# Performance work log

Hardware: AMD Instinct MI355X
Metric: run time of the kernel (lower is better)

Reference implementation:

```python
import jax, jax.numpy as jnp
import numpy as np

NUM_HEADS = 16
ROPE_THETA = 10000.0
SEQ = 2048
D_MODEL = 2048


def _rope(x):
    # x: (seq, heads, head_dim). Equinox RotaryPositionalEmbedding:
    # rotate_half variant with tiled (non-interleaved) cos/sin.
    S, H, hd = x.shape
    half = hd // 2
    freqs = 1.0 / (ROPE_THETA ** (jnp.arange(0, half, dtype=jnp.float32) * 2.0 / hd))  # (half,)
    t = jnp.arange(S, dtype=jnp.float32)
    angles = jnp.outer(t, freqs)  # (S, half)
    cos = jnp.tile(jnp.cos(angles), (1, 2))[:, None, :]  # (S, 1, hd)
    sin = jnp.tile(jnp.sin(angles), (1, 2))[:, None, :]
    x1, x2 = jnp.split(x, 2, axis=-1)
    rot = jnp.concatenate((-x2, x1), axis=-1)  # rotate_half
    return (x * cos + rot * sin).astype(x.dtype)


def setup_inputs() -> dict:
    key = jax.random.key(0)
    ks = jax.random.split(key, 7)
    mk = lambda k, scale=1.0: (jax.random.normal(k, (SEQ, D_MODEL), dtype=jnp.float32) * scale)
    return {
        "query": mk(ks[0]),
        "key_": mk(ks[1]),
        "value": mk(ks[2]),
        "Wq": jax.random.normal(ks[3], (D_MODEL, D_MODEL), dtype=jnp.float32) / np.sqrt(D_MODEL),
        "Wk": jax.random.normal(ks[4], (D_MODEL, D_MODEL), dtype=jnp.float32) / np.sqrt(D_MODEL),
        "Wv": jax.random.normal(ks[5], (D_MODEL, D_MODEL), dtype=jnp.float32) / np.sqrt(D_MODEL),
        "Wo": jax.random.normal(ks[6], (D_MODEL, D_MODEL), dtype=jnp.float32) / np.sqrt(D_MODEL),
    }


def reference(query, key_, value, Wq, Wk, Wv, Wo):
    S, D = query.shape
    H = NUM_HEADS
    hd = D // H
    # QKV projections (equinox Linear: y = W @ x, vmapped over seq -> x @ W.T)
    q = (query @ Wq.T).reshape(S, H, hd)
    k = (key_ @ Wk.T).reshape(S, H, hd)
    v = (value @ Wv.T).reshape(S, H, hd)
    # Per-head RoPE on q and k
    q = _rope(q)
    k = _rope(k)
    # Causal attention, scale 1/sqrt(head_dim) (dropout_p=0, inference)
    attn = jax.nn.dot_product_attention(q[None], k[None], v[None], is_causal=True)[0]  # (S, H, hd)
    # Output projection
    return attn.reshape(S, D) @ Wo.T
```

## Files before the change

kernel.cpp:

```cpp
#include <hip/hip_runtime.h>

typedef unsigned short u16;
typedef __attribute__((ext_vector_type(8))) __bf16 bf16x8;
typedef __attribute__((ext_vector_type(4))) float f32x4;

#define D_MODEL 2048
#define SEQ 2048
#define NHEAD 16
#define HDIM 128

#define AS1 __attribute__((address_space(1)))
#define AS3 __attribute__((address_space(3)))
#define GL2LDS(g, l) __builtin_amdgcn_global_load_lds((AS1 const void*)(g), (AS3 void*)(l), 16, 0, 0)

__device__ __forceinline__ u16 f2bf(float f) {
  unsigned u = __float_as_uint(f);
  u += 0x7fff + ((u >> 16) & 1);
  return (u16)(u >> 16);
}
__device__ __forceinline__ float bf2f(u16 h) {
  return __uint_as_float(((unsigned)h) << 16);
}
__device__ __forceinline__ float fexp2(float x) {
#if __has_builtin(__builtin_amdgcn_exp2f)
  return __builtin_amdgcn_exp2f(x);
#else
  return __expf(x * 0.69314718055994531f);
#endif
}

__global__ __launch_bounds__(256) void k_cast7(const float* i0, const float* i1, const float* i2,
                                               const float* i3, const float* i4, const float* i5,
                                               const float* i6,
                                               u16* o0, u16* o1, u16* o2, u16* o3, u16* o4,
                                               u16* o5, u16* o6) {
  const float* in; u16* out;
  switch (blockIdx.y) {
    case 0: in = i0; out = o0; break;
    case 1: in = i1; out = o1; break;
    case 2: in = i2; out = o2; break;
    case 3: in = i3; out = o3; break;
    case 4: in = i4; out = o4; break;
    case 5: in = i5; out = o5; break;
    default: in = i6; out = o6; break;
  }
  const int i = blockIdx.x * blockDim.x + threadIdx.x;
  const float4 v = reinterpret_cast<const float4*>(in)[i];
  ushort4 o;
  o.x = f2bf(v.x); o.y = f2bf(v.y); o.z = f2bf(v.z); o.w = f2bf(v.w);
  reinterpret_cast<ushort4*>(out)[i] = o;
}

__device__ __forceinline__ void stage128(const u16* __restrict__ P, u16* dst, int row0, int kt,
                                         int t, int w) {
#pragma unroll
  for (int c = 0; c < 4; ++c) {
    const int r = (c * 2048 + t * 8) >> 6;
    const int ch = ((t & 7) ^ (r & 7)) * 8;
    GL2LDS(P + (size_t)(row0 + r) * D_MODEL + kt + ch, dst + c * 2048 + w * 512);
  }
}
__device__ __forceinline__ void stage64(const u16* __restrict__ P, u16* dst, int row0, int kt,
                                        int t, int w) {
#pragma unroll
  for (int c = 0; c < 2; ++c) {
    const int r = (c * 2048 + t * 8) >> 6;
    const int ch = ((t & 7) ^ (r & 7)) * 8;
    GL2LDS(P + (size_t)(row0 + r) * D_MODEL + kt + ch, dst + c * 2048 + w * 512);
  }
}

__device__ __forceinline__ void gemm_nt_body(const u16* __restrict__ A, const u16* __restrict__ B,
                                             void* __restrict__ C, u16* As0, u16* As1,
                                             u16* Bs0, u16* Bs1, int outmode) {
  const int tn = blockIdx.x, tm = blockIdx.y;
  const int t = threadIdx.x;
  const int lane = t & 63, w = t >> 6;
  const int wr = w >> 1, wc = w & 1;
  const int lrow = lane & 15, g = lane >> 4;
  f32x4 acc[4][4] = {};

  stage128(A, As0, tm * 128, 0, t, w);
  stage128(B, Bs0, tn * 128, 0, t, w);
  __syncthreads();

  u16 *Ar = As0, *Br = Bs0, *Aw = As1, *Bw = Bs1;
#pragma unroll 1
  for (int kt = 0; kt < D_MODEL; kt += 64) {
    if (kt + 64 < D_MODEL) {
      stage128(A, Aw, tm * 128, kt + 64, t, w);
      stage128(B, Bw, tn * 128, kt + 64, t, w);
    }
#pragma unroll
    for (int kk = 0; kk < 2; ++kk) {
      bf16x8 af[4], bfr[4];
#pragma unroll
      for (int i = 0; i < 4; ++i) {
        const int sw = (((kk << 2) + g) ^ (lrow & 7)) * 8;
        af[i]  = *(const bf16x8*)(Ar + (wr * 64 + i * 16 + lrow) * 64 + sw);
        bfr[i] = *(const bf16x8*)(Br + (wc * 64 + i * 16 + lrow) * 64 + sw);
      }
#pragma unroll
      for (int i = 0; i < 4; ++i)
#pragma unroll
        for (int j = 0; j < 4; ++j)
          acc[i][j] = __builtin_amdgcn_mfma_f32_16x16x32_bf16(af[i], bfr[j], acc[i][j], 0, 0, 0);
    }
    __syncthreads();
    u16* tp;
    tp = Ar; Ar = Aw; Aw = tp;
    tp = Br; Br = Bw; Bw = tp;
  }

  const int crow0 = tm * 128 + wr * 64 + (lane >> 4) * 4;
  const int ccol0 = tn * 128 + wc * 64 + lrow;
  if (outmode == 2) {
#pragma unroll
    for (int i = 0; i < 4; ++i)
#pragma unroll
      for (int j = 0; j < 4; ++j) {
        ushort4 o;
        o.x = f2bf(acc[i][j][0]); o.y = f2bf(acc[i][j][1]);
        o.z = f2bf(acc[i][j][2]); o.w = f2bf(acc[i][j][3]);
        *(ushort4*)((u16*)C + (size_t)(ccol0 + j * 16) * D_MODEL + crow0 + i * 16) = o;
      }
  } else {
#pragma unroll
    for (int i = 0; i < 4; ++i)
#pragma unroll
      for (int j = 0; j < 4; ++j)
#pragma unroll
        for (int r = 0; r < 4; ++r)
          ((u16*)C)[(size_t)(crow0 + i * 16 + r) * D_MODEL + ccol0 + j * 16] = f2bf(acc[i][j][r]);
  }
}

__global__ __launch_bounds__(256, 2) void k_gemm_qkv(const u16* Xq, const u16* Xk, const u16* Xv,
                                                     const u16* Wq, const u16* Wk, const u16* Wv,
                                                     u16* Q, u16* K, u16* VT) {
  __shared__ u16 As[2][128 * 64], Bs[2][128 * 64];
  const int z = blockIdx.z;
  const u16* A = (z == 0) ? Xq : (z == 1) ? Xk : Xv;
  const u16* B = (z == 0) ? Wq : (z == 1) ? Wk : Wv;
  u16* C = (z == 0) ? Q : (z == 1) ? K : VT;
  gemm_nt_body(A, B, C, As[0], As[1], Bs[0], Bs[1], (z == 2) ? 2 : 0);
}

__global__ __launch_bounds__(256, 2) void k_gemm_out(const u16* __restrict__ A, const u16* __restrict__ B,
                                                     float* __restrict__ C) {
  __shared__ u16 As[2][128 * 64], Bs[2][64 * 64];
  const int tn = blockIdx.x, tm = blockIdx.y;
  const int t = threadIdx.x;
  const int lane = t & 63, w = t >> 6;
  const int wr = w >> 1, wc = w & 1;
  const int lrow = lane & 15, g = lane >> 4;
  f32x4 acc[4][2] = {};

  stage128(A, As[0], tm * 128, 0, t, w);
  stage64(B, Bs[0], tn * 64, 0, t, w);
  __syncthreads();

  u16 *Ar = As[0], *Br = Bs[0], *Aw = As[1], *Bw = Bs[1];
#pragma unroll 1
  for (int kt = 0; kt < D_MODEL; kt += 64) {
    if (kt + 64 < D_MODEL) {
      stage128(A, Aw, tm * 128, kt + 64, t, w);
      stage64(B, Bw, tn * 64, kt + 64, t, w);
    }
#pragma unroll
    for (int kk = 0; kk < 2; ++kk) {
      bf16x8 af[4], bfr[2];
#pragma unroll
      for (int i = 0; i < 4; ++i) {
        const int sw = (((kk << 2) + g) ^ (lrow & 7)) * 8;
        af[i] = *(const bf16x8*)(Ar + (wr * 64 + i * 16 + lrow) * 64 + sw);
        if (i < 2) bfr[i] = *(const bf16x8*)(Br + (wc * 32 + i * 16 + lrow) * 64 + sw);
      }
#pragma unroll
      for (int i = 0; i < 4; ++i)
#pragma unroll
        for (int j = 0; j < 2; ++j)
          acc[i][j] = __builtin_amdgcn_mfma_f32_16x16x32_bf16(af[i], bfr[j], acc[i][j], 0, 0, 0);
    }
    __syncthreads();
    u16* tp;
    tp = Ar; Ar = Aw; Aw = tp;
    tp = Br; Br = Bw; Bw = tp;
  }
  const int crow0 = tm * 128 + wr * 64 + (lane >> 4) * 4;
  const int ccol0 = tn * 64 + wc * 32 + lrow;
#pragma unroll
  for (int i = 0; i < 4; ++i)
#pragma unroll
    for (int j = 0; j < 2; ++j)
#pragma unroll
      for (int r = 0; r < 4; ++r)
        C[(size_t)(crow0 + i * 16 + r) * D_MODEL + ccol0 + j * 16] = acc[i][j][r];
}

__global__ __launch_bounds__(256) void k_rope(u16* Q, u16* K) {
  const int idx = blockIdx.x * blockDim.x + threadIdx.x;
  u16* X = blockIdx.y ? K : Q;
  const float scale = blockIdx.y ? 1.0f : (1.4426950408889634f * 0.08838834764831845f);
  const int s = idx >> 10;
  const int h = (idx >> 6) & 15;
  const int j = idx & 63;
  const float freq = __expf((float)j * -0.14391156831212787f);
  float sn, cs;
  sincosf((float)s * freq, &sn, &cs);
  const size_t base = (size_t)s * D_MODEL + h * HDIM + j;
  const float x1 = bf2f(X[base]), x2 = bf2f(X[base + 64]);
  X[base]      = f2bf((x1 * cs - x2 * sn) * scale);
  X[base + 64] = f2bf((x2 * cs + x1 * sn) * scale);
}

__global__ __launch_bounds__(256, 2) void k_attn(const u16* __restrict__ Q, const u16* __restrict__ K,
                                                 const u16* __restrict__ VT, u16* __restrict__ O) {
  __shared__ u16 Kb[2][64 * 128];
  __shared__ u16 Vb[2][128 * 64];
  __shared__ u16 Pl[4][32 * 64];
  const int bx = blockIdx.x;
  const int h = bx & 15;
  const int qt = 31 - (bx >> 4);
  const int t = threadIdx.x;
  const int lane = t & 63, w = t >> 6;
  const int mh = w & 1, par = w >> 1;
  const int lrow = lane & 15, g = lane >> 4, lk = g * 8;
  const int qrow0 = qt * 64 + mh * 32;

  bf16x8 qf[2][4];
#pragma unroll
  for (int mi = 0; mi < 2; ++mi)
#pragma unroll
    for (int ks = 0; ks < 4; ++ks)
      qf[mi][ks] = *(const bf16x8*)(Q + (size_t)(qrow0 + mi * 16 + lrow) * D_MODEL + h * HDIM + ks * 32 + lk);

  f32x4 accO[2][8] = {};
  float m_run[2][4], l_run[2][4];
#pragma unroll
  for (int mi = 0; mi < 2; ++mi)
#pragma unroll
    for (int r = 0; r < 4; ++r) { m_run[mi][r] = -1e30f; l_run[mi][r] = 0.f; }

  const int nt = qt + 1;
  const int nss = (nt + 1) >> 1;
#pragma unroll 1
  for (int s = 0; s < nss; ++s) {
    const int t0 = 2 * s;
    const int t1 = (2 * s + 1 < nt) ? 2 * s + 1 : nt - 1;
#pragma unroll
    for (int i = 0; i < 4; ++i) {
      const int rk = w * 16 + i * 4 + (lane >> 4);
      const int ck = lane & 15;
      GL2LDS(K + (size_t)(t0 * 64 + rk) * D_MODEL + h * HDIM + ((ck ^ (rk & 15)) * 8),
             Kb[0] + (w * 16 + i * 4) * 128);
      GL2LDS(K + (size_t)(t1 * 64 + rk) * D_MODEL + h * HDIM + ((ck ^ (rk & 15)) * 8),
             Kb[1] + (w * 16 + i * 4) * 128);
      const int rv = w * 32 + i * 8 + (lane >> 3);
      const int cv = lane & 7;
      GL2LDS(VT + (size_t)(h * HDIM + rv) * D_MODEL + t0 * 64 + ((cv ^ (rv & 7)) * 8),
             Vb[0] + (w * 32 + i * 8) * 64);
      GL2LDS(VT + (size_t)(h * HDIM + rv) * D_MODEL + t1 * 64 + ((cv ^ (rv & 7)) * 8),
             Vb[1] + (w * 32 + i * 8) * 64);
    }
    __syncthreads();

    const int T = 2 * s + par;
    if (T < nt) {
      f32x4 sc[2][4] = {};
#pragma unroll
      for (int ks = 0; ks < 4; ++ks) {
        bf16x8 kf[4];
#pragma unroll
        for (int ni = 0; ni < 4; ++ni)
          kf[ni] = *(const bf16x8*)(&Kb[par][(ni * 16 + lrow) * 128 + ((ks * 4 + g) ^ lrow) * 8]);
#pragma unroll
        for (int mi = 0; mi < 2; ++mi)
#pragma unroll
          for (int ni = 0; ni < 4; ++ni)
            sc[mi][ni] = __builtin_amdgcn_mfma_f32_16x16x32_bf16(qf[mi][ks], kf[ni], sc[mi][ni], 0, 0, 0);
      }

      if (T == qt) {
        const int kv = T * 64;
#pragma unroll
        for (int mi = 0; mi < 2; ++mi)
#pragma unroll
          for (int ni = 0; ni < 4; ++ni) {
            const int colg = kv + ni * 16 + lrow;
#pragma unroll
            for (int r = 0; r < 4; ++r) {
              const int rowg = qrow0 + mi * 16 + g * 4 + r;
              if (colg > rowg) sc[mi][ni][r] = -1e30f;
            }
          }
      }

#pragma unroll
      for (int mi = 0; mi < 2; ++mi)
#pragma unroll
        for (int r = 0; r < 4; ++r) {
          float pm = fmaxf(fmaxf(sc[mi][0][r], sc[mi][1][r]), fmaxf(sc[mi][2][r], sc[mi][3][r]));
          pm = fmaxf(pm, __shfl_xor(pm, 1));
          pm = fmaxf(pm, __shfl_xor(pm, 2));
          pm = fmaxf(pm, __shfl_xor(pm, 4));
          pm = fmaxf(pm, __shfl_xor(pm, 8));
          const float mo = m_run[mi][r];
          const float mn = fmaxf(mo, pm);
          const float sf = fexp2(mo - mn);
          float rs = 0.f;
#pragma unroll
          for (int ni = 0; ni < 4; ++ni) {
            const float p = fexp2(sc[mi][ni][r] - mn);
            sc[mi][ni][r] = p;
            rs += p;
          }
          rs += __shfl_xor(rs, 1);
          rs += __shfl_xor(rs, 2);
          rs += __shfl_xor(rs, 4);
          rs += __shfl_xor(rs, 8);
          l_run[mi][r] = l_run[mi][r] * sf + rs;
          m_run[mi][r] = mn;
#pragma unroll
          for (int dt = 0; dt < 8; ++dt) accO[mi][dt][r] *= sf;
        }

#pragma unroll
      for (int mi = 0; mi < 2; ++mi)
#pragma unroll
        for (int ni = 0; ni < 4; ++ni)
#pragma unroll
          for (int r = 0; r < 4; ++r) {
            const int row = mi * 16 + g * 4 + r;
            const int chnk = (2 * ni + (lrow >> 3)) ^ (row & 7);
            Pl[w][row * 64 + chnk * 8 + (lrow & 7)] = f2bf(sc[mi][ni][r]);
          }
      asm volatile("s_waitcnt lgkmcnt(0)" ::: "memory");

#pragma unroll
      for (int ks2 = 0; ks2 < 2; ++ks2) {
        bf16x8 pf[2];
#pragma unroll
        for (int mi = 0; mi < 2; ++mi) {
          const int row = mi * 16 + lrow;
          pf[mi] = *(const bf16x8*)(&Pl[w][row * 64 + ((ks2 * 4 + g) ^ (row & 7)) * 8]);
        }
#pragma unroll
        for (int dt = 0; dt < 8; ++dt) {
          const int R = dt * 16 + lrow;
          const bf16x8 vf = *(const bf16x8*)(&Vb[par][R * 64 + ((ks2 * 4 + g) ^ (R & 7)) * 8]);
#pragma unroll
          for (int mi = 0; mi < 2; ++mi)
            accO[mi][dt] = __builtin_amdgcn_mfma_f32_16x16x32_bf16(pf[mi], vf, accO[mi][dt], 0, 0, 0);
        }
      }
    }
    __syncthreads();
  }

  float* mrg = (float*)&Kb[0][0];
  float* mlb = (float*)&Vb[0][0];
  if (par == 1) {
#pragma unroll
    for (int mi = 0; mi < 2; ++mi)
#pragma unroll
      for (int dt = 0; dt < 8; ++dt)
#pragma unroll
        for (int r = 0; r < 4; ++r)
          mrg[mh * 4096 + (mi * 16 + g * 4 + r) * 128 + dt * 16 + lrow] = accO[mi][dt][r];
#pragma unroll
    for (int mi = 0; mi < 2; ++mi)
#pragma unroll
      for (int r = 0; r < 4; ++r) {
        const int row = mi * 16 + g * 4 + r;
        mlb[mh * 64 + row * 2]     = m_run[mi][r];
        mlb[mh * 64 + row * 2 + 1] = l_run[mi][r];
      }
  }
  __syncthreads();
  if (par == 0) {
#pragma unroll
    for (int mi = 0; mi < 2; ++mi)
#pragma unroll
      for (int r = 0; r < 4; ++r) {
        const int row = mi * 16 + g * 4 + r;
        const float m1 = mlb[mh * 64 + row * 2];
        const float l1 = mlb[mh * 64 + row * 2 + 1];
        const float mn = fmaxf(m_run[mi][r], m1);
        const float f0 = fexp2(m_run[mi][r] - mn);
        const float f1 = fexp2(m1 - mn);
        const float inv = 1.0f / (l_run[mi][r] * f0 + l1 * f1);
        const size_t grow = (size_t)(qrow0 + row);
#pragma unroll
        for (int dt = 0; dt < 8; ++dt) {
          const float v1 = mrg[mh * 4096 + row * 128 + dt * 16 + lrow];
          O[grow * D_MODEL + h * HDIM + dt * 16 + lrow] =
              f2bf((accO[mi][dt][r] * f0 + v1 * f1) * inv);
        }
      }
  }
}

extern "C" void kernel_launch(void* const* d_in, const int* in_sizes, int n_in,
                              void* d_out, int out_size, void* d_ws, size_t ws_size,
                              hipStream_t stream) {
  const float* query = (const float*)d_in[0];
  const float* key_  = (const float*)d_in[1];
  const float* value = (const float*)d_in[2];
  const float* Wq    = (const float*)d_in[3];
  const float* Wk    = (const float*)d_in[4];
  const float* Wv    = (const float*)d_in[5];
  const float* Wo    = (const float*)d_in[6];
  float* out = (float*)d_out;

  const size_t TS = (size_t)SEQ * D_MODEL;
  u16* ws  = (u16*)d_ws;
  u16* bXq = ws + 0 * TS;
  u16* bXk = ws + 1 * TS;
  u16* bXv = ws + 2 * TS;
  u16* bWq = ws + 3 * TS;
  u16* bWk = ws + 4 * TS;
  u16* bWv = ws + 5 * TS;
  u16* bWo = ws + 6 * TS;
  u16* bQ  = ws + 7 * TS;
  u16* bK  = ws + 8 * TS;
  u16* bVT = ws + 9 * TS;
  u16* bA  = ws + 10 * TS;

  const int n4 = (int)(TS / 4);
  k_cast7<<<dim3(n4 / 256, 7), 256, 0, stream>>>(query, key_, value, Wq, Wk, Wv, Wo,
                                                 bXq, bXk, bXv, bWq, bWk, bWv, bWo);

  k_gemm_qkv<<<dim3(16, 16, 3), 256, 0, stream>>>(bXq, bXk, bXv, bWq, bWk, bWv, bQ, bK, bVT);

  k_rope<<<dim3((SEQ * NHEAD * 64) / 256, 2), 256, 0, stream>>>(bQ, bK);

  k_attn<<<dim3(512), 256, 0, stream>>>(bQ, bK, bVT, bA);

  k_gemm_out<<<dim3(32, 16), 256, 0, stream>>>(bA, bWo, out);
}
```

Measured before the change: 310.2 us.

## Pair causal query tiles per block, double-buffer K/V, and defer softmax rescale

Each attention block now processes two query tiles (pj and 31-pj), which balances causal work, and the grid is halved to 256 blocks. K/V tiles are double-buffered in LDS so the next stage's global-to-LDS loads are issued before the current stage's compute. The online softmax skips the running-max update and accumulator rescale when the new row max exceeds the old by at most 8 (log2 domain) across the whole wave. LDS use doubles to about 144KB, which limits residency to one block per CU and leaves only 256 blocks on a GPU with many CUs. The deferred rescale lets probabilities grow up to 2^8 before renormalizing, which costs some bf16 precision headroom.

```diff
diff --git a/kernel.cpp b/kernel.cpp
--- a/kernel.cpp
+++ b/kernel.cpp
@@ -214,190 +214,210 @@
   X[base + 64] = f2bf((x2 * cs + x1 * sn) * scale);
 }
 
-__global__ __launch_bounds__(256, 2) void k_attn(const u16* __restrict__ Q, const u16* __restrict__ K,
-                                                 const u16* __restrict__ VT, u16* __restrict__ O) {
-  __shared__ u16 Kb[2][64 * 128];
-  __shared__ u16 Vb[2][128 * 64];
+__global__ __launch_bounds__(256) void k_attn(const u16* __restrict__ Q, const u16* __restrict__ K,
+                                              const u16* __restrict__ VT, u16* __restrict__ O) {
+  __shared__ u16 Kb[2][2][64 * 128];
+  __shared__ u16 Vb[2][2][128 * 64];
   __shared__ u16 Pl[4][32 * 64];
   const int bx = blockIdx.x;
   const int h = bx & 15;
-  const int qt = 31 - (bx >> 4);
+  const int pj = bx >> 4;
   const int t = threadIdx.x;
   const int lane = t & 63, w = t >> 6;
   const int mh = w & 1, par = w >> 1;
   const int lrow = lane & 15, g = lane >> 4, lk = g * 8;
-  const int qrow0 = qt * 64 + mh * 32;
-
-  bf16x8 qf[2][4];
-#pragma unroll
-  for (int mi = 0; mi < 2; ++mi)
-#pragma unroll
-    for (int ks = 0; ks < 4; ++ks)
-      qf[mi][ks] = *(const bf16x8*)(Q + (size_t)(qrow0 + mi * 16 + lrow) * D_MODEL + h * HDIM + ks * 32 + lk);
-
-  f32x4 accO[2][8] = {};
-  float m_run[2][4], l_run[2][4];
-#pragma unroll
-  for (int mi = 0; mi < 2; ++mi)
-#pragma unroll
-    for (int r = 0; r < 4; ++r) { m_run[mi][r] = -1e30f; l_run[mi][r] = 0.f; }
-
-  const int nt = qt + 1;
-  const int nss = (nt + 1) >> 1;
-#pragma unroll 1
-  for (int s = 0; s < nss; ++s) {
-    const int t0 = 2 * s;
-    const int t1 = (2 * s + 1 < nt) ? 2 * s + 1 : nt - 1;
+
+  auto STAGE = [&](int b, int ss, int nt2) {
+    const int t0 = 2 * ss;
+    const int t1 = (2 * ss + 1 < nt2) ? 2 * ss + 1 : nt2 - 1;
 #pragma unroll
     for (int i = 0; i < 4; ++i) {
       const int rk = w * 16 + i * 4 + (lane >> 4);
       const int ck = lane & 15;
       GL2LDS(K + (size_t)(t0 * 64 + rk) * D_MODEL + h * HDIM + ((ck ^ (rk & 15)) * 8),
-             Kb[0] + (w * 16 + i * 4) * 128);
+             Kb[b][0] + (w * 16 + i * 4) * 128);
       GL2LDS(K + (size_t)(t1 * 64 + rk) * D_MODEL + h * HDIM + ((ck ^ (rk & 15)) * 8),
-             Kb[1] + (w * 16 + i * 4) * 128);
+             Kb[b][1] + (w * 16 + i * 4) * 128);
       const int rv = w * 32 + i * 8 + (lane >> 3);
       const int cv = lane & 7;
       GL2LDS(VT + (size_t)(h * HDIM + rv) * D_MODEL + t0 * 64 + ((cv ^ (rv & 7)) * 8),
-             Vb[0] + (w * 32 + i * 8) * 64);
+             Vb[b][0] + (w * 32 + i * 8) * 64);
       GL2LDS(VT + (size_t)(h * HDIM + rv) * D_MODEL + t1 * 64 + ((cv ^ (rv & 7)) * 8),
-             Vb[1] + (w * 32 + i * 8) * 64);
-    }
+             Vb[b][1] + (w * 32 + i * 8) * 64);
+    }
+  };
+
+  int cur = 0;
+#pragma unroll 1
+  for (int side = 0; side < 2; ++side) {
+    const int qt = side ? (31 - pj) : pj;
+    const int nt = qt + 1;
+    const int nss = (nt + 1) >> 1;
+    const int qrow0 = qt * 64 + mh * 32;
+
+    bf16x8 qf[2][4];
+#pragma unroll
+    for (int mi = 0; mi < 2; ++mi)
+#pragma unroll
+      for (int ks = 0; ks < 4; ++ks)
+        qf[mi][ks] = *(const bf16x8*)(Q + (size_t)(qrow0 + mi * 16 + lrow) * D_MODEL + h * HDIM + ks * 32 + lk);
+
+    f32x4 accO[2][8] = {};
+    float m_run[2][4], l_run[2][4];
+#pragma unroll
+    for (int mi = 0; mi < 2; ++mi)
+#pragma unroll
+      for (int r = 0; r < 4; ++r) { m_run[mi][r] = -1e30f; l_run[mi][r] = 0.f; }
+
+    STAGE(cur, 0, nt);
     __syncthreads();
 
-    const int T = 2 * s + par;
-    if (T < nt) {
-      f32x4 sc[2][4] = {};
-#pragma unroll
-      for (int ks = 0; ks < 4; ++ks) {
-        bf16x8 kf[4];
-#pragma unroll
-        for (int ni = 0; ni < 4; ++ni)
-          kf[ni] = *(const bf16x8*)(&Kb[par][(ni * 16 + lrow) * 128 + ((ks * 4 + g) ^ lrow) * 8]);
+#pragma unroll 1
+    for (int ss = 0; ss < nss; ++ss) {
+      if (ss + 1 < nss) STAGE(cur ^ 1, ss + 1, nt);
+
+      const int T = 2 * ss + par;
+      if (T < nt) {
+        f32x4 sc[2][4] = {};
+#pragma unroll
+        for (int ks = 0; ks < 4; ++ks) {
+          bf16x8 kf[4];
+#pragma unroll
+          for (int ni = 0; ni < 4; ++ni)
+            kf[ni] = *(const bf16x8*)(&Kb[cur][par][(ni * 16 + lrow) * 128 + ((ks * 4 + g) ^ lrow) * 8]);
+#pragma unroll
+          for (int mi = 0; mi < 2; ++mi)
+#pragma unroll
+            for (int ni = 0; ni < 4; ++ni)
+              sc[mi][ni] = __builtin_amdgcn_mfma_f32_16x16x32_bf16(qf[mi][ks], kf[ni], sc[mi][ni], 0, 0, 0);
+        }
+
+        if (T == qt) {
+          const int kv = T * 64;
+#pragma unroll
+          for (int mi = 0; mi < 2; ++mi)
+#pragma unroll
+            for (int ni = 0; ni < 4; ++ni) {
+              const int colg = kv + ni * 16 + lrow;
+#pragma unroll
+              for (int r = 0; r < 4; ++r) {
+                const int rowg = qrow0 + mi * 16 + g * 4 + r;
+                if (colg > rowg) sc[mi][ni][r] = -1e30f;
+              }
+            }
+        }
+
 #pragma unroll
         for (int mi = 0; mi < 2; ++mi)
 #pragma unroll
-          for (int ni = 0; ni < 4; ++ni)
-            sc[mi][ni] = __builtin_amdgcn_mfma_f32_16x16x32_bf16(qf[mi][ks], kf[ni], sc[mi][ni], 0, 0, 0);
-      }
-
-      if (T == qt) {
-        const int kv = T * 64;
-#pragma unroll
-        for (int mi = 0; mi < 2; ++mi)
-#pragma unroll
-          for (int ni = 0; ni < 4; ++ni) {
-            const int colg = kv + ni * 16 + lrow;
-#pragma unroll
-            for (int r = 0; r < 4; ++r) {
-              const int rowg = qrow0 + mi * 16 + g * 4 + r;
-              if (colg > rowg) sc[mi][ni][r] = -1e30f;
+          for (int r = 0; r < 4; ++r) {
+            float pm = fmaxf(fmaxf(sc[mi][0][r], sc[mi][1][r]), fmaxf(sc[mi][2][r], sc[mi][3][r]));
+            pm = fmaxf(pm, __shfl_xor(pm, 1));
+            pm = fmaxf(pm, __shfl_xor(pm, 2));
+            pm = fmaxf(pm, __shfl_xor(pm, 4));
+            pm = fmaxf(pm, __shfl_xor(pm, 8));
+            const float mo = m_run[mi][r];
+            const bool defer = __all(pm - mo <= 8.f);
+            float base = mo, sf = 1.0f;
+            if (!defer) {
+              base = fmaxf(mo, pm);
+              sf = fexp2(mo - base);
+              m_run[mi][r] = base;
+            }
+            float rs = 0.f;
+#pragma unroll
+            for (int ni = 0; ni < 4; ++ni) {
+              const float p = fexp2(sc[mi][ni][r] - base);
+              sc[mi][ni][r] = p;
+              rs += p;
+            }
+            rs += __shfl_xor(rs, 1);
+            rs += __shfl_xor(rs, 2);
+            rs += __shfl_xor(rs, 4);
+            rs += __shfl_xor(rs, 8);
+            l_run[mi][r] = fmaf(l_run[mi][r], sf, rs);
+            if (!defer) {
+#pragma unroll
+              for (int dt = 0; dt < 8; ++dt) accO[mi][dt][r] *= sf;
             }
           }
-      }
-
-#pragma unroll
-      for (int mi = 0; mi < 2; ++mi)
-#pragma unroll
-        for (int r = 0; r < 4; ++r) {
-          float pm = fmaxf(fmaxf(sc[mi][0][r], sc[mi][1][r]), fmaxf(sc[mi][2][r], sc[mi][3][r]));
-          pm = fmaxf(pm, __shfl_xor(pm, 1));
-          pm = fmaxf(pm, __shfl_xor(pm, 2));
-          pm = fmaxf(pm, __shfl_xor(pm, 4));
-          pm = fmaxf(pm, __shfl_xor(pm, 8));
-          const float mo = m_run[mi][r];
-          const float mn = fmaxf(mo, pm);
-          const float sf = fexp2(mo - mn);
-          float rs = 0.f;
-#pragma unroll
-          for (int ni = 0; ni < 4; ++ni) {
-            const float p = fexp2(sc[mi][ni][r] - mn);
-            sc[mi][ni][r] = p;
-            rs += p;
+
+#pragma unroll
+        for (int mi = 0; mi < 2; ++mi)
+#pragma unroll
+          for (int ni = 0; ni < 4; ++ni)
+#pragma unroll
+            for (int r = 0; r < 4; ++r) {
+              const int row = mi * 16 + g * 4 + r;
+              const int chnk = (2 * ni + (lrow >> 3)) ^ (row & 7);
+              Pl[w][row * 64 + chnk * 8 + (lrow & 7)] = f2bf(sc[mi][ni][r]);
+            }
+        asm volatile("s_waitcnt lgkmcnt(0)" ::: "memory");
+
+#pragma unroll
+        for (int ks2 = 0; ks2 < 2; ++ks2) {
+          bf16x8 pf[2];
+#pragma unroll
+          for (int mi = 0; mi < 2; ++mi) {
+            const int row = mi * 16 + lrow;
+            pf[mi] = *(const bf16x8*)(&Pl[w][row * 64 + ((ks2 * 4 + g) ^ (row & 7)) * 8]);
           }
-          rs += __shfl_xor(rs, 1);
-          rs += __shfl_xor(rs, 2);
-          rs += __shfl_xor(rs, 4);
-          rs += __shfl_xor(rs, 8);
-          l_run[mi][r] = l_run[mi][r] * sf + rs;
-          m_run[mi][r] = mn;
-#pragma unroll
-          for (int dt = 0; dt < 8; ++dt) accO[mi][dt][r] *= sf;
-        }
-
-#pragma unroll
-      for (int mi = 0; mi < 2; ++mi)
-#pragma unroll
-        for (int ni = 0; ni < 4; ++ni)
-#pragma unroll
-          for (int r = 0; r < 4; ++r) {
-            const int row = mi * 16 + g * 4 + r;
-            const int chnk = (2 * ni + (lrow >> 3)) ^ (row & 7);
-            Pl[w][row * 64 + chnk * 8 + (lrow & 7)] = f2bf(sc[mi][ni][r]);
+#pragma unroll
+          for (int dt = 0; dt < 8; ++dt) {
+            const int R = dt * 16 + lrow;
+            const bf16x8 vf = *(const bf16x8*)(&Vb[cur][par][R * 64 + ((ks2 * 4 + g) ^ (R & 7)) * 8]);
+#pragma unroll
+            for (int mi = 0; mi < 2; ++mi)
+              accO[mi][dt] = __builtin_amdgcn_mfma_f32_16x16x32_bf16(pf[mi], vf, accO[mi][dt], 0, 0, 0);
           }
-      asm volatile("s_waitcnt lgkmcnt(0)" ::: "memory");
-
-#pragma unroll
-      for (int ks2 = 0; ks2 < 2; ++ks2) {
-        bf16x8 pf[2];
-#pragma unroll
-        for (int mi = 0; mi < 2; ++mi) {
-          const int row = mi * 16 + lrow;
-          pf[mi] = *(const bf16x8*)(&Pl[w][row * 64 + ((ks2 * 4 + g) ^ (row & 7)) * 8]);
-        }
-#pragma unroll
-        for (int dt = 0; dt < 8; ++dt) {
-          const int R = dt * 16 + lrow;
-          const bf16x8 vf = *(const bf16x8*)(&Vb[par][R * 64 + ((ks2 * 4 + g) ^ (R & 7)) * 8]);
-#pragma unroll
-          for (int mi = 0; mi < 2; ++mi)
-            accO[mi][dt] = __builtin_amdgcn_mfma_f32_16x16x32_bf16(pf[mi], vf, accO[mi][dt], 0, 0, 0);
         }
       }
+      __syncthreads();
+      cur ^= 1;
+    }
+
+    float* mrg = (float*)&Kb[0][0][0];
+    float* mlb = (float*)&Vb[0][0][0];
+    if (par == 1) {
+#pragma unroll
+      for (int mi = 0; mi < 2; ++mi)
+#pragma unroll
+        for (int dt = 0; dt < 8; ++dt)
+#pragma unroll
+          for (int r = 0; r < 4; ++r)
+            mrg[mh * 4096 + (mi * 16 + g * 4 + r) * 128 + dt * 16 + lrow] = accO[mi][dt][r];
+#pragma unroll
+      for (int mi = 0; mi < 2; ++mi)
+#pragma unroll
+        for (int r = 0; r < 4; ++r) {
+          const int row = mi * 16 + g * 4 + r;
+          mlb[mh * 64 + row * 2]     = m_run[mi][r];
+          mlb[mh * 64 + row * 2 + 1] = l_run[mi][r];
+        }
     }
     __syncthreads();
-  }
-
-  float* mrg = (float*)&Kb[0][0];
-  float* mlb = (float*)&Vb[0][0];
-  if (par == 1) {
-#pragma unroll
-    for (int mi = 0; mi < 2; ++mi)
-#pragma unroll
-      for (int dt = 0; dt < 8; ++dt)
-#pragma unroll
-        for (int r = 0; r < 4; ++r)
-          mrg[mh * 4096 + (mi * 16 + g * 4 + r) * 128 + dt * 16 + lrow] = accO[mi][dt][r];
-#pragma unroll
-    for (int mi = 0; mi < 2; ++mi)
-#pragma unroll
-      for (int r = 0; r < 4; ++r) {
-        const int row = mi * 16 + g * 4 + r;
-        mlb[mh * 64 + row * 2]     = m_run[mi][r];
-        mlb[mh * 64 + row * 2 + 1] = l_run[mi][r];
-      }
-  }
-  __syncthreads();
-  if (par == 0) {
-#pragma unroll
-    for (int mi = 0; mi < 2; ++mi)
-#pragma unroll
-      for (int r = 0; r < 4; ++r) {
-        const int row = mi * 16 + g * 4 + r;
-        const float m1 = mlb[mh * 64 + row * 2];
-        const float l1 = mlb[mh * 64 + row * 2 + 1];
-        const float mn = fmaxf(m_run[mi][r], m1);
-        const float f0 = fexp2(m_run[mi][r] - mn);
-        const float f1 = fexp2(m1 - mn);
-        const float inv = 1.0f / (l_run[mi][r] * f0 + l1 * f1);
-        const size_t grow = (size_t)(qrow0 + row);
-#pragma unroll
-        for (int dt = 0; dt < 8; ++dt) {
-          const float v1 = mrg[mh * 4096 + row * 128 + dt * 16 + lrow];
-          O[grow * D_MODEL + h * HDIM + dt * 16 + lrow] =
-              f2bf((accO[mi][dt][r] * f0 + v1 * f1) * inv);
+    if (par == 0) {
+#pragma unroll
+      for (int mi = 0; mi < 2; ++mi)
+#pragma unroll
+        for (int r = 0; r < 4; ++r) {
+          const int row = mi * 16 + g * 4 + r;
+          const float m1 = mlb[mh * 64 + row * 2];
+          const float l1 = mlb[mh * 64 + row * 2 + 1];
+          const float mn = fmaxf(m_run[mi][r], m1);
+          const float f0 = fexp2(m_run[mi][r] - mn);
+          const float f1 = fexp2(m1 - mn);
+          const float inv = 1.0f / (l_run[mi][r] * f0 + l1 * f1);
+          const size_t grow = (size_t)(qrow0 + row);
+#pragma unroll
+          for (int dt = 0; dt < 8; ++dt) {
+            const float v1 = mrg[mh * 4096 + row * 128 + dt * 16 + lrow];
+            O[grow * D_MODEL + h * HDIM + dt * 16 + lrow] =
+                f2bf((accO[mi][dt][r] * f0 + v1 * f1) * inv);
+          }
         }
-      }
+    }
+    __syncthreads();
   }
 }
 
@@ -435,7 +455,7 @@
 
   k_rope<<<dim3((SEQ * NHEAD * 64) / 256, 2), 256, 0, stream>>>(bQ, bK);
 
-  k_attn<<<dim3(512), 256, 0, stream>>>(bQ, bK, bVT, bA);
+  k_attn<<<dim3(256), 256, 0, stream>>>(bQ, bK, bVT, bA);
 
   k_gemm_out<<<dim3(32, 16), 256, 0, stream>>>(bA, bWo, out);
 }
```

New measurement: 343.0 us. +10.6%, slower.
